# Optimization experiments

Hardware: AMD Instinct MI355X
Metric: run time of the kernel (lower is better)

## Reference

```python
import jax, jax.numpy as jnp
import numpy as np

EMB = 64      # embedding_dim
HID = 128     # hidden_dim
SCALE = 4.0   # InputEmbedding scale
N_TRACKS = 32768


def lstm_cell(x, h, c, W_ih, W_hh, b_ih, b_hh):
    # torch.nn.LSTMCell gate order: i, f, g, o
    gates = x @ W_ih.T + b_ih + h @ W_hh.T + b_hh  # [N, 4*HID]
    i, f, g, o = jnp.split(gates, 4, axis=-1)
    i = jax.nn.sigmoid(i)
    f = jax.nn.sigmoid(f)
    g = jnp.tanh(g)
    o = jax.nn.sigmoid(o)
    c_new = f * c + i * g
    h_new = o * jnp.tanh(c_new)
    return h_new, c_new


def setup_inputs() -> dict:
    key = jax.random.key(0)
    ks = jax.random.split(key, 14)

    def init(k, shape, fan_in):
        b = 1.0 / np.sqrt(fan_in)
        return jax.random.uniform(k, shape, jnp.float32, -b, b)

    return {
        "observed": jax.random.normal(ks[0], (9, N_TRACKS, 2), jnp.float32),
        "prediction": jax.random.normal(ks[1], (12, N_TRACKS, 2), jnp.float32),
        # InputEmbedding: Linear(2, EMB-2) followed by ReLU, 2 tag dims appended
        "W_emb": init(ks[2], (EMB - 2, 2), 2),
        "b_emb": init(ks[3], (EMB - 2,), 2),
        # LSTMCell(EMB, HID)
        "W_ih": init(ks[4], (4 * HID, EMB), HID),
        "W_hh": init(ks[5], (4 * HID, HID), HID),
        "b_ih": init(ks[6], (4 * HID,), HID),
        "b_hh": init(ks[7], (4 * HID,), HID),
        # real_classifier MLP: 128 -> 64 -> 32 -> 1, ReLU after each Linear
        "W1": init(ks[8], (HID // 2, HID), HID),
        "b1": init(ks[9], (HID // 2,), HID),
        "W2": init(ks[10], (HID // 4, HID // 2), HID // 2),
        "b2": init(ks[11], (HID // 4,), HID // 2),
        "W3": init(ks[12], (1, HID // 4), HID // 4),
        "b3": init(ks[13], (1,), HID // 4),
    }


def reference(observed, prediction, W_emb, b_emb, W_ih, W_hh, b_ih, b_hh,
              W1, b1, W2, b2, W3, b3):
    seq = jnp.concatenate([observed, prediction], axis=0)  # [T, N, 2]
    N = seq.shape[1]
    h = jnp.zeros((N, HID), seq.dtype)
    c = jnp.zeros((N, HID), seq.dtype)

    # tag_step: start_enc tag is one-hot at position EMB-2
    tag = jnp.zeros((N, EMB), seq.dtype).at[:, EMB - 2].set(1.0)
    h, c = lstm_cell(tag, h, c, W_ih, W_hh, b_ih, b_hh)

    def step(carry, xs):
        h, c = carry
        obs1, obs2 = xs
        # track visible iff both frames are non-NaN
        mask = ~(jnp.isnan(obs1[:, 0]) | jnp.isnan(obs2[:, 0]))  # [N]
        vel = jnp.where(mask[:, None], obs2 - obs1, 0.0)
        emb = jax.nn.relu((vel * SCALE) @ W_emb.T + b_emb)       # [N, EMB-2]
        emb = jnp.concatenate([emb, jnp.zeros((N, 2), emb.dtype)], axis=1)
        h_new, c_new = lstm_cell(emb, h, c, W_ih, W_hh, b_ih, b_hh)
        # scatter updated states back only for visible tracks
        h = jnp.where(mask[:, None], h_new, h)
        c = jnp.where(mask[:, None], c_new, c)
        return (h, c), None

    (h, c), _ = jax.lax.scan(step, (h, c), (seq[:-1], seq[1:]))

    # real_classifier applied to hidden state of track 0
    x = jax.nn.relu(h[0] @ W1.T + b1)
    x = jax.nn.relu(x @ W2.T + b2)
    scores = jax.nn.relu(x @ W3.T + b3)  # shape (1,)
    return scores
```

## Files before the change

kernel.cpp:

```cpp
#include <hip/hip_runtime.h>
#include <math.h>

#define NT 32768
#define SCALEF 4.0f

typedef _Float16 h2v __attribute__((ext_vector_type(2)));

__device__ __forceinline__ unsigned rlu(unsigned u, int l) {
    return (unsigned)__builtin_amdgcn_readlane((int)u, l);
}

__device__ __forceinline__ unsigned pk2(float lo, float hi) {
    unsigned a = (unsigned)__builtin_bit_cast(unsigned short, (_Float16)lo);
    unsigned b = (unsigned)__builtin_bit_cast(unsigned short, (_Float16)hi);
    return a | (b << 16);
}
__device__ __forceinline__ float upk_lo(unsigned u) {
    return (float)__builtin_bit_cast(_Float16, (unsigned short)(u & 0xffffu));
}

__device__ __forceinline__ float dot2(unsigned w, unsigned h, float acc) {
#if defined(__has_builtin) && __has_builtin(__builtin_amdgcn_fdot2)
    return __builtin_amdgcn_fdot2(__builtin_bit_cast(h2v, w),
                                  __builtin_bit_cast(h2v, h), acc, false);
#else
    float r = fmaf(upk_lo(w), upk_lo(h), acc);
    return fmaf((float)__builtin_bit_cast(_Float16, (unsigned short)(w >> 16)),
                (float)__builtin_bit_cast(_Float16, (unsigned short)(h >> 16)), r);
#endif
}

__device__ __forceinline__ float sigf(float x) {
    return __builtin_amdgcn_rcpf(1.0f + __expf(-x));
}
__device__ __forceinline__ float tanhfast(float x) {
    return 1.0f - 2.0f * __builtin_amdgcn_rcpf(1.0f + __expf(2.0f * x));
}

__device__ __forceinline__ float frame_val(const float* __restrict__ obs,
                                           const float* __restrict__ pred,
                                           int F, int d) {
    return (F < 9) ? obs[F * (NT * 2) + d] : pred[(F - 9) * (NT * 2) + d];
}

__attribute__((amdgpu_waves_per_eu(4, 4)))
__global__ void __launch_bounds__(1024) lstm_disc_kernel(
                                 const float* __restrict__ observed,
                                 const float* __restrict__ prediction,
                                 const float* __restrict__ W_emb,
                                 const float* __restrict__ b_emb,
                                 const float* __restrict__ W_ih,
                                 const float* __restrict__ W_hh,
                                 const float* __restrict__ b_ih,
                                 const float* __restrict__ b_hh,
                                 const float* __restrict__ W1,
                                 const float* __restrict__ b1,
                                 const float* __restrict__ W2,
                                 const float* __restrict__ b2,
                                 const float* __restrict__ W3,
                                 const float* __restrict__ b3,
                                 float* __restrict__ out)
{
    const int tid  = (int)threadIdx.x;
    const int lane = tid & 63;
    const int j    = tid & 511;
    const int p    = tid >> 9;

    __shared__ uint4    whh4[8 * 1024];
    __shared__ unsigned xs_pk[21 * 32];
    __shared__ float    ppart[1024];
    __shared__ unsigned hpk[64];
    __shared__ float    hfin[128];
    __shared__ float    velx[21], vely[21], maskf[21];
    __shared__ float    mlp1[64], mlp2[32];

    if (tid < 20) {
        float ax = frame_val(observed, prediction, tid,     0);
        float ay = frame_val(observed, prediction, tid,     1);
        float bx = frame_val(observed, prediction, tid + 1, 0);
        float by = frame_val(observed, prediction, tid + 1, 1);
        unsigned ua = __float_as_uint(ax) & 0x7fffffffu;
        unsigned ub = __float_as_uint(bx) & 0x7fffffffu;
        bool m = !((ua > 0x7f800000u) || (ub > 0x7f800000u));
        maskf[tid + 1] = m ? 1.0f : 0.0f;
        velx[tid + 1]  = m ? (bx - ax) * SCALEF : 0.0f;
        vely[tid + 1]  = m ? (by - ay) * SCALEF : 0.0f;
    }
    if (tid == 20) { maskf[0] = 1.0f; velx[0] = 0.0f; vely[0] = 0.0f; }

    unsigned xw[16];
    {
        const float4* Wi = reinterpret_cast<const float4*>(W_ih + j * 64 + 32 * p);
        #pragma unroll
        for (int q = 0; q < 8; ++q) {
            float4 w = Wi[q];
            xw[2 * q]     = pk2(w.x, w.y);
            xw[2 * q + 1] = pk2(w.z, w.w);
        }
    }
    const float bias = b_ih[j] + b_hh[j];

    __syncthreads();

    unsigned short* xs16 = (unsigned short*)xs_pk;
    for (int idx = tid; idx < 21 * 64; idx += 1024) {
        int s = idx >> 6, e = idx & 63;
        float v;
        if (s == 0)      v = (e == 62) ? 1.0f : 0.0f;
        else if (e < 62) v = fmaxf(velx[s] * W_emb[2 * e] + vely[s] * W_emb[2 * e + 1] + b_emb[e], 0.0f);
        else             v = 0.0f;
        xs16[s * 64 + e] = __builtin_bit_cast(unsigned short, (_Float16)v);
    }

    {
        const float4* Wh = reinterpret_cast<const float4*>(W_hh + j * 128 + 64 * p);
        #pragma unroll
        for (int g = 0; g < 8; ++g) {
            float4 wa = Wh[2 * g], wb = Wh[2 * g + 1];
            uint4 u;
            u.x = pk2(wa.x, wa.y); u.y = pk2(wa.z, wa.w);
            u.z = pk2(wb.x, wb.y); u.w = pk2(wb.z, wb.w);
            whh4[g * 1024 + tid] = u;
        }
    }

    unsigned mbits = 0;
    #pragma unroll
    for (int s = 0; s < 21; ++s) mbits |= (maskf[s] != 0.0f ? 1u : 0u) << s;

    __syncthreads();

    float gxr[21];
    gxr[0] = (p == 0) ? bias : upk_lo(xw[15]);
    #pragma unroll
    for (int s = 1; s < 21; ++s) {
        unsigned xp = xs_pk[s * 32 + 16 * p + (lane & 15)];
        float a0 = (p == 0) ? bias : 0.0f, a1 = 0.0f;
        #pragma unroll
        for (int q = 0; q < 16; ++q) {
            if (q & 1) a1 = dot2(xw[q], rlu(xp, q), a1);
            else       a0 = dot2(xw[q], rlu(xp, q), a0);
        }
        gxr[s] = a0 + a1;
    }

    uint4 w0 = whh4[0 * 1024 + tid], w1 = whh4[1 * 1024 + tid];
    uint4 w2 = whh4[2 * 1024 + tid], w3 = whh4[3 * 1024 + tid];
    uint4 w4 = whh4[4 * 1024 + tid], w5 = whh4[5 * 1024 + tid];
    uint4 w6 = whh4[6 * 1024 + tid], w7 = whh4[7 * 1024 + tid];

    unsigned short* hpk16 = (unsigned short*)hpk;
    float creg = 0.0f;
    unsigned hp = 0u;
    #pragma unroll
    for (int s = 0; s < 21; ++s) {
        if (mbits & (1u << s)) {
            float a0 = gxr[s], a1 = 0.0f;
            a0 = dot2(w0.x, rlu(hp,  0), a0); a1 = dot2(w0.y, rlu(hp,  1), a1);
            a0 = dot2(w0.z, rlu(hp,  2), a0); a1 = dot2(w0.w, rlu(hp,  3), a1);
            a0 = dot2(w1.x, rlu(hp,  4), a0); a1 = dot2(w1.y, rlu(hp,  5), a1);
            a0 = dot2(w1.z, rlu(hp,  6), a0); a1 = dot2(w1.w, rlu(hp,  7), a1);
            a0 = dot2(w2.x, rlu(hp,  8), a0); a1 = dot2(w2.y, rlu(hp,  9), a1);
            a0 = dot2(w2.z, rlu(hp, 10), a0); a1 = dot2(w2.w, rlu(hp, 11), a1);
            a0 = dot2(w3.x, rlu(hp, 12), a0); a1 = dot2(w3.y, rlu(hp, 13), a1);
            a0 = dot2(w3.z, rlu(hp, 14), a0); a1 = dot2(w3.w, rlu(hp, 15), a1);
            a0 = dot2(w4.x, rlu(hp, 16), a0); a1 = dot2(w4.y, rlu(hp, 17), a1);
            a0 = dot2(w4.z, rlu(hp, 18), a0); a1 = dot2(w4.w, rlu(hp, 19), a1);
            a0 = dot2(w5.x, rlu(hp, 20), a0); a1 = dot2(w5.y, rlu(hp, 21), a1);
            a0 = dot2(w5.z, rlu(hp, 22), a0); a1 = dot2(w5.w, rlu(hp, 23), a1);
            a0 = dot2(w6.x, rlu(hp, 24), a0); a1 = dot2(w6.y, rlu(hp, 25), a1);
            a0 = dot2(w6.z, rlu(hp, 26), a0); a1 = dot2(w6.w, rlu(hp, 27), a1);
            a0 = dot2(w7.x, rlu(hp, 28), a0); a1 = dot2(w7.y, rlu(hp, 29), a1);
            a0 = dot2(w7.z, rlu(hp, 30), a0); a1 = dot2(w7.w, rlu(hp, 31), a1);
            ppart[tid] = a0 + a1;
            __syncthreads();
            if (tid < 128) {
                float gi = sigf(    ppart[tid      ] + ppart[512 + tid]);
                float gf = sigf(    ppart[128 + tid] + ppart[640 + tid]);
                float gg = tanhfast(ppart[256 + tid] + ppart[768 + tid]);
                float go = sigf(    ppart[384 + tid] + ppart[896 + tid]);
                creg = fmaf(gf, creg, gi * gg);
                float hv = go * tanhfast(creg);
                hfin[tid] = hv;
                hpk16[tid] = __builtin_bit_cast(unsigned short, (_Float16)hv);
            }
            __syncthreads();
            hp = hpk[32 * p + (lane & 31)];
        }
    }

    if (tid < 64) {
        const float4* W1r = reinterpret_cast<const float4*>(W1 + tid * 128);
        float a = b1[tid];
        #pragma unroll
        for (int q = 0; q < 32; ++q) {
            float4 w = W1r[q];
            a = fmaf(w.x, hfin[4*q], a);   a = fmaf(w.y, hfin[4*q+1], a);
            a = fmaf(w.z, hfin[4*q+2], a); a = fmaf(w.w, hfin[4*q+3], a);
        }
        mlp1[tid] = fmaxf(a, 0.0f);
    }
    __syncthreads();
    if (tid < 32) {
        const float4* W2r = reinterpret_cast<const float4*>(W2 + tid * 64);
        float a = b2[tid];
        #pragma unroll
        for (int q = 0; q < 16; ++q) {
            float4 w = W2r[q];
            a = fmaf(w.x, mlp1[4*q], a);   a = fmaf(w.y, mlp1[4*q+1], a);
            a = fmaf(w.z, mlp1[4*q+2], a); a = fmaf(w.w, mlp1[4*q+3], a);
        }
        mlp2[tid] = fmaxf(a, 0.0f);
    }
    __syncthreads();
    if (tid == 0) {
        float a = b3[0];
        #pragma unroll
        for (int k = 0; k < 32; ++k) a += W3[k] * mlp2[k];
        out[0] = fmaxf(a, 0.0f);
    }
}

extern "C" void kernel_launch(void* const* d_in, const int* in_sizes, int n_in,
                              void* d_out, int out_size, void* d_ws, size_t ws_size,
                              hipStream_t stream) {
    lstm_disc_kernel<<<1, 1024, 0, stream>>>(
        (const float*)d_in[0],  (const float*)d_in[1],
        (const float*)d_in[2],  (const float*)d_in[3],
        (const float*)d_in[4],  (const float*)d_in[5],
        (const float*)d_in[6],  (const float*)d_in[7],
        (const float*)d_in[8],  (const float*)d_in[9],
        (const float*)d_in[10], (const float*)d_in[11],
        (const float*)d_in[12], (const float*)d_in[13],
        (float*)d_out);
}
```

Before: 117.7 us.

## Precompute input-gate projections into shared fp16 table and keep recurrent loop rolled

Stops keeping 21 per-thread input-projection values in registers. Instead the two partial sums are reduced through shared memory and stored as fp16 in a shared table indexed by step and gate. The recurrent loop is no longer unrolled, and an empty asm statement keeps the W_hh weights pinned in VGPRs, cutting register pressure and code size. In exchange it adds 42 block barriers during precompute, an LDS load per step, and fp16 rounding of the input gate contributions.

```diff
diff --git a/kernel.cpp b/kernel.cpp
--- a/kernel.cpp
+++ b/kernel.cpp
@@ -5,6 +5,7 @@
 #define SCALEF 4.0f
 
 typedef _Float16 h2v __attribute__((ext_vector_type(2)));
+typedef unsigned uvec4 __attribute__((ext_vector_type(4)));
 
 __device__ __forceinline__ unsigned rlu(unsigned u, int l) {
     return (unsigned)__builtin_amdgcn_readlane((int)u, l);
@@ -42,6 +43,9 @@
                                            int F, int d) {
     return (F < 9) ? obs[F * (NT * 2) + d] : pred[(F - 9) * (NT * 2) + d];
 }
+
+#define PIN8(a,b,c,d,e,f,g,h) \
+    asm("" : "+v"(a), "+v"(b), "+v"(c), "+v"(d), "+v"(e), "+v"(f), "+v"(g), "+v"(h))
 
 __attribute__((amdgpu_waves_per_eu(4, 4)))
 __global__ void __launch_bounds__(1024) lstm_disc_kernel(
@@ -66,13 +70,14 @@
     const int j    = tid & 511;
     const int p    = tid >> 9;
 
-    __shared__ uint4    whh4[8 * 1024];
-    __shared__ unsigned xs_pk[21 * 32];
-    __shared__ float    ppart[1024];
-    __shared__ unsigned hpk[64];
-    __shared__ float    hfin[128];
-    __shared__ float    velx[21], vely[21], maskf[21];
-    __shared__ float    mlp1[64], mlp2[32];
+    __shared__ uvec4          whh4[8 * 1024];
+    __shared__ unsigned short gxu16[21 * 512];
+    __shared__ float          ppart[1024];
+    __shared__ unsigned       xs_pk[21 * 32];
+    __shared__ unsigned       hpk[64];
+    __shared__ float          hfin[128];
+    __shared__ float          velx[21], vely[21], maskf[21];
+    __shared__ float          mlp1[64], mlp2[32];
 
     if (tid < 20) {
         float ax = frame_val(observed, prediction, tid,     0);
@@ -117,7 +122,7 @@
         #pragma unroll
         for (int g = 0; g < 8; ++g) {
             float4 wa = Wh[2 * g], wb = Wh[2 * g + 1];
-            uint4 u;
+            uvec4 u;
             u.x = pk2(wa.x, wa.y); u.y = pk2(wa.z, wa.w);
             u.z = pk2(wb.x, wb.y); u.w = pk2(wb.z, wb.w);
             whh4[g * 1024 + tid] = u;
@@ -130,32 +135,42 @@
 
     __syncthreads();
 
-    float gxr[21];
-    gxr[0] = (p == 0) ? bias : upk_lo(xw[15]);
-    #pragma unroll
-    for (int s = 1; s < 21; ++s) {
-        unsigned xp = xs_pk[s * 32 + 16 * p + (lane & 15)];
-        float a0 = (p == 0) ? bias : 0.0f, a1 = 0.0f;
-        #pragma unroll
-        for (int q = 0; q < 16; ++q) {
-            if (q & 1) a1 = dot2(xw[q], rlu(xp, q), a1);
-            else       a0 = dot2(xw[q], rlu(xp, q), a0);
-        }
-        gxr[s] = a0 + a1;
-    }
-
-    uint4 w0 = whh4[0 * 1024 + tid], w1 = whh4[1 * 1024 + tid];
-    uint4 w2 = whh4[2 * 1024 + tid], w3 = whh4[3 * 1024 + tid];
-    uint4 w4 = whh4[4 * 1024 + tid], w5 = whh4[5 * 1024 + tid];
-    uint4 w6 = whh4[6 * 1024 + tid], w7 = whh4[7 * 1024 + tid];
+    for (int s = 0; s < 21; ++s) {
+        float hv;
+        if (s == 0) {
+            hv = (p == 0) ? bias : upk_lo(xw[15]);
+        } else {
+            unsigned xp = xs_pk[s * 32 + 16 * p + (lane & 15)];
+            float a0 = (p == 0) ? bias : 0.0f, a1 = 0.0f;
+            #pragma unroll
+            for (int q = 0; q < 16; ++q) {
+                if (q & 1) a1 = dot2(xw[q], rlu(xp, q), a1);
+                else       a0 = dot2(xw[q], rlu(xp, q), a0);
+            }
+            hv = a0 + a1;
+        }
+        ppart[tid] = hv;
+        __syncthreads();
+        if (tid < 512)
+            gxu16[s * 512 + tid] =
+                __builtin_bit_cast(unsigned short, (_Float16)(ppart[tid] + ppart[512 + tid]));
+        __syncthreads();
+    }
+
+    uvec4 w0 = whh4[0 * 1024 + tid], w1 = whh4[1 * 1024 + tid];
+    uvec4 w2 = whh4[2 * 1024 + tid], w3 = whh4[3 * 1024 + tid];
+    uvec4 w4 = whh4[4 * 1024 + tid], w5 = whh4[5 * 1024 + tid];
+    uvec4 w6 = whh4[6 * 1024 + tid], w7 = whh4[7 * 1024 + tid];
 
     unsigned short* hpk16 = (unsigned short*)hpk;
     float creg = 0.0f;
     unsigned hp = 0u;
-    #pragma unroll
+    #pragma unroll 1
     for (int s = 0; s < 21; ++s) {
         if (mbits & (1u << s)) {
-            float a0 = gxr[s], a1 = 0.0f;
+            PIN8(w0, w1, w2, w3, w4, w5, w6, w7);
+            float gxv = (float)__builtin_bit_cast(_Float16, gxu16[s * 512 + j]);
+            float a0 = gxv, a1 = 0.0f;
             a0 = dot2(w0.x, rlu(hp,  0), a0); a1 = dot2(w0.y, rlu(hp,  1), a1);
             a0 = dot2(w0.z, rlu(hp,  2), a0); a1 = dot2(w0.w, rlu(hp,  3), a1);
             a0 = dot2(w1.x, rlu(hp,  4), a0); a1 = dot2(w1.y, rlu(hp,  5), a1);
```

Result: no change. 115.6 us (-1.8%).
